# Optimization experiments

Hardware: AMD Instinct MI355X
Metric: run time of the kernel (lower is better)

## Reference

```python
import jax, jax.numpy as jnp
import numpy as np

N_NODES = 100000
EPS_BN = 1e-5


def setup_inputs() -> dict:
    key = jax.random.key(0)
    k1, k2, k3, k4, k5, k6 = jax.random.split(key, 6)
    x = jax.random.normal(k1, (N_NODES, 200), dtype=jnp.float32)
    edge_index = jax.random.randint(k2, (2, 1600000), 0, N_NODES, dtype=jnp.int64)
    # GCNConv params (Glorot-ish scale)
    W = jax.random.normal(k3, (200, 64), dtype=jnp.float32) * (1.0 / np.sqrt(200.0))
    b = jax.random.normal(k4, (64,), dtype=jnp.float32) * 0.01
    # BatchNorm1d affine params
    bn_weight = jax.random.normal(k5, (64,), dtype=jnp.float32) * 0.1 + 1.0
    bn_bias = jax.random.normal(k6, (64,), dtype=jnp.float32) * 0.1
    return {"x": x, "edge_index": edge_index, "W": W, "b": b,
            "bn_weight": bn_weight, "bn_bias": bn_bias}


def _gcn_conv(x, edge_index, W, b):
    n = x.shape[0]
    # linear transform first (PyG GCNConv order): [N, 64]
    xw = x @ W
    # add self-loops
    loop = jnp.arange(n, dtype=edge_index.dtype)
    src = jnp.concatenate([edge_index[0], loop])
    dst = jnp.concatenate([edge_index[1], loop])
    # symmetric normalization: deg over dst (incl. self loops)
    deg = jax.ops.segment_sum(jnp.ones_like(dst, dtype=xw.dtype), dst, num_segments=n)
    dinv = jnp.where(deg > 0, jax.lax.rsqrt(deg), 0.0)
    norm = dinv[src] * dinv[dst]  # [E+N]
    # gather-scale-scatter: out[dst] += norm * xw[src]
    msg = xw[src] * norm[:, None]
    out = jax.ops.segment_sum(msg, dst, num_segments=n)
    return out + b


def reference(x, edge_index, W, b, bn_weight, bn_bias):
    h = _gcn_conv(x, edge_index, W, b)
    h = jax.nn.relu(h)
    # BatchNorm1d in training mode: biased batch statistics over nodes
    mean = jnp.mean(h, axis=0)
    var = jnp.mean(jnp.square(h - mean), axis=0)
    y = (h - mean) * jax.lax.rsqrt(var + EPS_BN) * bn_weight + bn_bias
    return y
```

## Files before the change

### kernel.cpp

```cpp
#include <hip/hip_runtime.h>

#define N_NODES 100000
#define N_EDGES 1600000
#define K_DIM   200
#define C_DIM   64
#define EPS_BN  1e-5f
#define MT      128
#define NKB     25
#define SLICE_U ((size_t)N_NODES * 16)
#define NPX     12500
#define MAXD    48

typedef int      vi4 __attribute__((ext_vector_type(4)));
typedef float    vf4 __attribute__((ext_vector_type(4)));
typedef unsigned vu4 __attribute__((ext_vector_type(4)));

__device__ __forceinline__ ushort f2bf(float f) {
    unsigned u = __float_as_uint(f);
    u = (u + 0x7FFFu + ((u >> 16) & 1u)) >> 16;
    return (ushort)u;
}

__global__ __launch_bounds__(256) void k_fillslot(
        const int* __restrict__ src, const int* __restrict__ dst,
        int* __restrict__ cursor, int* __restrict__ slot) {
    unsigned lo = (blockIdx.x & 7) * NPX;
    int i0 = (blockIdx.x >> 3) * 256 + threadIdx.x;
    int stride = (gridDim.x >> 3) * 256;
    for (int i = i0; i < N_EDGES / 4; i += stride) {
        vi4 d = ((const vi4*)dst)[i];
        vi4 s = ((const vi4*)src)[i];
        bool mx = (unsigned)(d.x - lo) < NPX;
        bool my = (unsigned)(d.y - lo) < NPX;
        bool mz = (unsigned)(d.z - lo) < NPX;
        bool mw = (unsigned)(d.w - lo) < NPX;
        if (mx) { int p = atomicAdd(&cursor[d.x], 1); if (p < MAXD) slot[(size_t)p * N_NODES + d.x] = s.x; }
        if (my) { int p = atomicAdd(&cursor[d.y], 1); if (p < MAXD) slot[(size_t)p * N_NODES + d.y] = s.y; }
        if (mz) { int p = atomicAdd(&cursor[d.z], 1); if (p < MAXD) slot[(size_t)p * N_NODES + d.z] = s.z; }
        if (mw) { int p = atomicAdd(&cursor[d.w], 1); if (p < MAXD) slot[(size_t)p * N_NODES + d.w] = s.w; }
    }
}

__global__ __launch_bounds__(256) void k_gemm2(const float* __restrict__ x,
                                               const float* __restrict__ W,
                                               const int* __restrict__ cursor,
                                               ushort* __restrict__ xsp) {
    __shared__ float xT[8][MT];
    __shared__ float Wt[8][C_DIM];
    int tid = threadIdx.x;
    int tx = tid & 15;
    int ty = tid >> 4;
    int row0 = blockIdx.x * MT;

    int lrow = tid >> 1;
    int lk   = (tid & 1) * 4;
    int grow = row0 + lrow;
    if (grow > N_NODES - 1) grow = N_NODES - 1;
    const float* xp = x + (size_t)grow * K_DIM + lk;
    int wk = tid >> 4;
    int wc = (tid & 15) * 4;

    float acc[8][4];
    #pragma unroll
    for (int i = 0; i < 8; ++i)
        #pragma unroll
        for (int j = 0; j < 4; ++j) acc[i][j] = 0.f;

    float4 xr = *(const float4*)xp;
    float4 wr = {0,0,0,0};
    if (tid < 128) wr = *(const float4*)(W + wk * C_DIM + wc);

    for (int kb = 0; kb < NKB; ++kb) {
        xT[lk + 0][lrow] = xr.x;
        xT[lk + 1][lrow] = xr.y;
        xT[lk + 2][lrow] = xr.z;
        xT[lk + 3][lrow] = xr.w;
        if (tid < 128) *(float4*)&Wt[wk][wc] = wr;
        __syncthreads();
        if (kb < NKB - 1) {
            xr = *(const float4*)(xp + (kb + 1) * 8);
            if (tid < 128) wr = *(const float4*)(W + ((kb + 1) * 8 + wk) * C_DIM + wc);
        }
        #pragma unroll
        for (int k = 0; k < 8; ++k) {
            float4 xa = *(const float4*)&xT[k][ty * 8];
            float4 xb = *(const float4*)&xT[k][ty * 8 + 4];
            float4 wv = *(const float4*)&Wt[k][tx * 4];
            float xv[8] = {xa.x, xa.y, xa.z, xa.w, xb.x, xb.y, xb.z, xb.w};
            #pragma unroll
            for (int i = 0; i < 8; ++i) {
                acc[i][0] = fmaf(xv[i], wv.x, acc[i][0]);
                acc[i][1] = fmaf(xv[i], wv.y, acc[i][1]);
                acc[i][2] = fmaf(xv[i], wv.z, acc[i][2]);
                acc[i][3] = fmaf(xv[i], wv.w, acc[i][3]);
            }
        }
        __syncthreads();
    }
    int sl  = tx >> 2;
    int pos = (tx & 3) * 4;
    #pragma unroll
    for (int i = 0; i < 8; ++i) {
        int r = row0 + ty * 8 + i;
        if (r < N_NODES) {
            float dv = rsqrtf((float)cursor[r] + 1.0f);
            ushort4 o = {f2bf(acc[i][0] * dv), f2bf(acc[i][1] * dv),
                         f2bf(acc[i][2] * dv), f2bf(acc[i][3] * dv)};
            *(ushort4*)(xsp + (size_t)sl * SLICE_U + (size_t)r * 16 + pos) = o;
        }
    }
}

#define UNPK0(u, k) { acc[k] = __uint_as_float((u) << 16); \
                      acc[k+1] = __uint_as_float((u) & 0xFFFF0000u); }
#define UNPKA(u, k) { acc[k] += __uint_as_float((u) << 16); \
                      acc[k+1] += __uint_as_float((u) & 0xFFFF0000u); }
#define ROWACC(aa, cc) { UNPKA(aa.x, 0)  UNPKA(aa.y, 2)  UNPKA(aa.z, 4)  UNPKA(aa.w, 6) \
                         UNPKA(cc.x, 8)  UNPKA(cc.y, 10) UNPKA(cc.z, 12) UNPKA(cc.w, 14) }

__global__ __launch_bounds__(256) void k_gath4(
        const int* __restrict__ slot, const int* __restrict__ cursor,
        const ushort* __restrict__ xsp, const float* __restrict__ b,
        ushort* __restrict__ hp2, float* __restrict__ stats) {
    int tid  = threadIdx.x;
    int lane = tid & 63;
    int widx = tid >> 6;
    int bid  = blockIdx.x;
    int slice = (bid & 7) >> 1;
    int chunk = ((bid >> 3) * 2 + (bid & 1)) * 4 + widx;
    int nchunks = (gridDim.x >> 3) * 8;
    const ushort* xs = xsp + (size_t)slice * SLICE_U;
    const float*  bs = b + slice * 16;
    float s1[16], s2[16];
    #pragma unroll
    for (int i = 0; i < 16; ++i) { s1[i] = 0.f; s2[i] = 0.f; }

    for (int n0 = chunk * 64; n0 < N_NODES; n0 += nchunks * 64) {
        int n = n0 + lane;
        bool act = n < N_NODES;
        int dg = 0;
        float dn = 0.f;
        float acc[16];
        if (act) {
            dg = __builtin_nontemporal_load(cursor + n);
            dn = rsqrtf((float)dg + 1.0f);
            if (dg > MAXD) dg = MAXD;
            const uint4* rp = (const uint4*)(xs + (size_t)n * 16);
            uint4 a = rp[0], c = rp[1];
            UNPK0(a.x, 0)  UNPK0(a.y, 2)  UNPK0(a.z, 4)  UNPK0(a.w, 6)
            UNPK0(c.x, 8)  UNPK0(c.y, 10) UNPK0(c.z, 12) UNPK0(c.w, 14)
        } else {
            #pragma unroll
            for (int i = 0; i < 16; ++i) acc[i] = 0.f;
        }
        const int* sp = slot + n;
        int p = 0;
        for (; p + 4 <= dg; p += 4) {
            int e0 = sp[(size_t)(p + 0) * N_NODES];
            int e1 = sp[(size_t)(p + 1) * N_NODES];
            int e2 = sp[(size_t)(p + 2) * N_NODES];
            int e3 = sp[(size_t)(p + 3) * N_NODES];
            const uint4* q0 = (const uint4*)(xs + (size_t)e0 * 16);
            const uint4* q1 = (const uint4*)(xs + (size_t)e1 * 16);
            const uint4* q2 = (const uint4*)(xs + (size_t)e2 * 16);
            const uint4* q3 = (const uint4*)(xs + (size_t)e3 * 16);
            uint4 a0 = q0[0], c0 = q0[1];
            uint4 a1 = q1[0], c1 = q1[1];
            uint4 a2 = q2[0], c2 = q2[1];
            uint4 a3 = q3[0], c3 = q3[1];
            ROWACC(a0, c0)  ROWACC(a1, c1)  ROWACC(a2, c2)  ROWACC(a3, c3)
        }
        for (; p + 2 <= dg; p += 2) {
            int e0 = sp[(size_t)(p + 0) * N_NODES];
            int e1 = sp[(size_t)(p + 1) * N_NODES];
            const uint4* q0 = (const uint4*)(xs + (size_t)e0 * 16);
            const uint4* q1 = (const uint4*)(xs + (size_t)e1 * 16);
            uint4 a0 = q0[0], c0 = q0[1];
            uint4 a1 = q1[0], c1 = q1[1];
            ROWACC(a0, c0)  ROWACC(a1, c1)
        }
        if (p < dg) {
            int e0 = sp[(size_t)p * N_NODES];
            const uint4* q0 = (const uint4*)(xs + (size_t)e0 * 16);
            uint4 a0 = q0[0], c0 = q0[1];
            ROWACC(a0, c0)
        }
        if (act) {
            unsigned pk[8];
            #pragma unroll
            for (int i2 = 0; i2 < 8; ++i2) {
                float lo = fmaxf(fmaf(dn, acc[2*i2+0], bs[2*i2+0]), 0.f);
                float hi = fmaxf(fmaf(dn, acc[2*i2+1], bs[2*i2+1]), 0.f);
                s1[2*i2+0] += lo; s2[2*i2+0] = fmaf(lo, lo, s2[2*i2+0]);
                s1[2*i2+1] += hi; s2[2*i2+1] = fmaf(hi, hi, s2[2*i2+1]);
                pk[i2] = (unsigned)f2bf(lo) | ((unsigned)f2bf(hi) << 16);
            }
            vu4 w0 = {pk[0], pk[1], pk[2], pk[3]};
            vu4 w1 = {pk[4], pk[5], pk[6], pk[7]};
            ushort* hb = hp2 + ((size_t)slice * N_NODES + (size_t)n) * 16;
            __builtin_nontemporal_store(w0, (vu4*)hb);
            __builtin_nontemporal_store(w1, (vu4*)(hb + 8));
        }
    }

    __shared__ float red[4][32];
    #pragma unroll
    for (int i = 0; i < 16; ++i) {
        float a = s1[i], c = s2[i];
        #pragma unroll
        for (int m = 1; m <= 32; m <<= 1) {
            a += __shfl_xor(a, m);
            c += __shfl_xor(c, m);
        }
        if (lane == 0) { red[widx][i] = a; red[widx][16 + i] = c; }
    }
    __syncthreads();
    if (tid < 32) {
        float v = red[0][tid] + red[1][tid] + red[2][tid] + red[3][tid];
        int ch = slice * 16 + (tid & 15);
        unsafeAtomicAdd(&stats[(tid >> 4) * 64 + ch], v);
    }
}

__global__ __launch_bounds__(256) void k_final_p(
        const ushort* __restrict__ hp2, const float* __restrict__ stats,
        const float* __restrict__ bnw, const float* __restrict__ bnb,
        float* __restrict__ out) {
    int tid = blockIdx.x * 256 + threadIdx.x;
    if (tid >= N_NODES * 8) return;
    int half = tid & 7;
    int n    = tid >> 3;
    int slice = half >> 1, sub = half & 1;
    int cb = slice * 16 + sub * 8;
    float sc[8], sh[8];
    #pragma unroll
    for (int j = 0; j < 8; ++j) {
        int c = cb + j;
        float mean = stats[c] * (1.0f / N_NODES);
        float var  = stats[64 + c] * (1.0f / N_NODES) - mean * mean;
        float s = rsqrtf(var + EPS_BN) * bnw[c];
        sc[j] = s;
        sh[j] = bnb[c] - mean * s;
    }
    vu4 v = __builtin_nontemporal_load(
        (const vu4*)(hp2 + ((size_t)slice * N_NODES + (size_t)n) * 16 + sub * 8));
    vf4 h0, h1;
    h0.x = __uint_as_float(v.x << 16); h0.y = __uint_as_float(v.x & 0xFFFF0000u);
    h0.z = __uint_as_float(v.y << 16); h0.w = __uint_as_float(v.y & 0xFFFF0000u);
    h1.x = __uint_as_float(v.z << 16); h1.y = __uint_as_float(v.z & 0xFFFF0000u);
    h1.z = __uint_as_float(v.w << 16); h1.w = __uint_as_float(v.w & 0xFFFF0000u);
    vf4 o0, o1;
    o0.x = fmaf(h0.x, sc[0], sh[0]); o0.y = fmaf(h0.y, sc[1], sh[1]);
    o0.z = fmaf(h0.z, sc[2], sh[2]); o0.w = fmaf(h0.w, sc[3], sh[3]);
    o1.x = fmaf(h1.x, sc[4], sh[4]); o1.y = fmaf(h1.y, sc[5], sh[5]);
    o1.z = fmaf(h1.z, sc[6], sh[6]); o1.w = fmaf(h1.w, sc[7], sh[7]);
    float* op = out + (size_t)n * C_DIM + cb;
    __builtin_nontemporal_store(o0, (vf4*)op);
    __builtin_nontemporal_store(o1, (vf4*)(op + 4));
}

extern "C" void kernel_launch(void* const* d_in, const int* in_sizes, int n_in,
                              void* d_out, int out_size, void* d_ws, size_t ws_size,
                              hipStream_t stream) {
    const float* x   = (const float*)d_in[0];
    const int*   ei  = (const int*)d_in[1];
    const float* W   = (const float*)d_in[2];
    const float* b   = (const float*)d_in[3];
    const float* bnw = (const float*)d_in[4];
    const float* bnb = (const float*)d_in[5];
    float* out = (float*)d_out;

    const int* src = ei;
    const int* dst = ei + N_EDGES;
    char* ws = (char*)d_ws;

    const size_t SZ_I = 400128;
    const size_t OFF_STAT = SZ_I;
    const size_t OFF_SLOT = SZ_I + 512;
    const size_t OFF_H    = OFF_SLOT + (size_t)N_NODES * MAXD * 4;
    const size_t ZERO_B   = SZ_I + 512;

    ushort* xsp = (ushort*)out;
    const int GEMM_GRID = (N_NODES + MT - 1) / MT;

    int*    cursor = (int*)ws;
    float*  stats  = (float*)(ws + OFF_STAT);
    int*    slot   = (int*)(ws + OFF_SLOT);
    ushort* hp2    = (ushort*)(ws + OFF_H);

    hipMemsetAsync(d_ws, 0, ZERO_B, stream);

    k_fillslot <<<2048, 256, 0, stream>>>(src, dst, cursor, slot);
    k_gemm2    <<<GEMM_GRID, 256, 0, stream>>>(x, W, cursor, xsp);
    k_gath4    <<<3136, 256, 0, stream>>>(slot, cursor, xsp, b, hp2, stats);
    k_final_p  <<<(N_NODES * 8 + 255) / 256, 256, 0, stream>>>(hp2, stats, bnw, bnb, out);
    (void)ws_size;
}
```

Baseline: 201.3 us.

## Fuse edge-slot fill and GEMM into one launch, apply source dinv in gather

The edge-bucketing fill and the x@W GEMM now run as disjoint block ranges of a single kernel, so the compute-bound GEMM can overlap the atomic-heavy fill. This is possible because the GEMM no longer scales rows by the source degree normalization. That scaling moves into the gather, which reads a per-node dinv array built by a new small kernel. The GEMM tile shrinks to 64 rows to give more blocks. The cost is an extra launch plus one extra dinv load and an FMA per gathered edge in the gather.

```diff
diff --git a/kernel.cpp b/kernel.cpp
--- a/kernel.cpp
+++ b/kernel.cpp
@@ -5,11 +5,13 @@
 #define K_DIM   200
 #define C_DIM   64
 #define EPS_BN  1e-5f
-#define MT      128
 #define NKB     25
 #define SLICE_U ((size_t)N_NODES * 16)
 #define NPX     12500
 #define MAXD    48
+#define NFILL   2048
+#define MTG     64
+#define NGEMM   ((N_NODES + MTG - 1) / MTG)
 
 typedef int      vi4 __attribute__((ext_vector_type(4)));
 typedef float    vf4 __attribute__((ext_vector_type(4)));
@@ -21,74 +23,74 @@
     return (ushort)u;
 }
 
-__global__ __launch_bounds__(256) void k_fillslot(
+__global__ __launch_bounds__(256, 8) void k_fillgemm(
         const int* __restrict__ src, const int* __restrict__ dst,
-        int* __restrict__ cursor, int* __restrict__ slot) {
-    unsigned lo = (blockIdx.x & 7) * NPX;
-    int i0 = (blockIdx.x >> 3) * 256 + threadIdx.x;
-    int stride = (gridDim.x >> 3) * 256;
-    for (int i = i0; i < N_EDGES / 4; i += stride) {
-        vi4 d = ((const vi4*)dst)[i];
-        vi4 s = ((const vi4*)src)[i];
-        bool mx = (unsigned)(d.x - lo) < NPX;
-        bool my = (unsigned)(d.y - lo) < NPX;
-        bool mz = (unsigned)(d.z - lo) < NPX;
-        bool mw = (unsigned)(d.w - lo) < NPX;
-        if (mx) { int p = atomicAdd(&cursor[d.x], 1); if (p < MAXD) slot[(size_t)p * N_NODES + d.x] = s.x; }
-        if (my) { int p = atomicAdd(&cursor[d.y], 1); if (p < MAXD) slot[(size_t)p * N_NODES + d.y] = s.y; }
-        if (mz) { int p = atomicAdd(&cursor[d.z], 1); if (p < MAXD) slot[(size_t)p * N_NODES + d.z] = s.z; }
-        if (mw) { int p = atomicAdd(&cursor[d.w], 1); if (p < MAXD) slot[(size_t)p * N_NODES + d.w] = s.w; }
-    }
-}
-
-__global__ __launch_bounds__(256) void k_gemm2(const float* __restrict__ x,
-                                               const float* __restrict__ W,
-                                               const int* __restrict__ cursor,
-                                               ushort* __restrict__ xsp) {
-    __shared__ float xT[8][MT];
+        int* __restrict__ cursor, int* __restrict__ slot,
+        const float* __restrict__ x, const float* __restrict__ W,
+        ushort* __restrict__ xsp) {
+    __shared__ float xT[8][MTG];
     __shared__ float Wt[8][C_DIM];
+    int bid = blockIdx.x;
     int tid = threadIdx.x;
+
+    if (bid < NFILL) {
+        unsigned lo = (bid & 7) * NPX;
+        int i0 = (bid >> 3) * 256 + tid;
+        int stride = (NFILL >> 3) * 256;
+        for (int i = i0; i < N_EDGES / 4; i += stride) {
+            vi4 d = ((const vi4*)dst)[i];
+            vi4 s = ((const vi4*)src)[i];
+            bool mx = (unsigned)(d.x - lo) < NPX;
+            bool my = (unsigned)(d.y - lo) < NPX;
+            bool mz = (unsigned)(d.z - lo) < NPX;
+            bool mw = (unsigned)(d.w - lo) < NPX;
+            if (mx) { int p = atomicAdd(&cursor[d.x], 1); if (p < MAXD) slot[(size_t)p * N_NODES + d.x] = s.x; }
+            if (my) { int p = atomicAdd(&cursor[d.y], 1); if (p < MAXD) slot[(size_t)p * N_NODES + d.y] = s.y; }
+            if (mz) { int p = atomicAdd(&cursor[d.z], 1); if (p < MAXD) slot[(size_t)p * N_NODES + d.z] = s.z; }
+            if (mw) { int p = atomicAdd(&cursor[d.w], 1); if (p < MAXD) slot[(size_t)p * N_NODES + d.w] = s.w; }
+        }
+        return;
+    }
+
+    int gbid = bid - NFILL;
+    int row0 = gbid * MTG;
     int tx = tid & 15;
     int ty = tid >> 4;
-    int row0 = blockIdx.x * MT;
-
-    int lrow = tid >> 1;
-    int lk   = (tid & 1) * 4;
+
+    int lrow = tid >> 2;
+    int lk   = (tid & 3) * 2;
     int grow = row0 + lrow;
     if (grow > N_NODES - 1) grow = N_NODES - 1;
     const float* xp = x + (size_t)grow * K_DIM + lk;
     int wk = tid >> 4;
     int wc = (tid & 15) * 4;
 
-    float acc[8][4];
-    #pragma unroll
-    for (int i = 0; i < 8; ++i)
+    float acc[4][4];
+    #pragma unroll
+    for (int i = 0; i < 4; ++i)
         #pragma unroll
         for (int j = 0; j < 4; ++j) acc[i][j] = 0.f;
 
-    float4 xr = *(const float4*)xp;
+    float2 xr = *(const float2*)xp;
     float4 wr = {0,0,0,0};
     if (tid < 128) wr = *(const float4*)(W + wk * C_DIM + wc);
 
     for (int kb = 0; kb < NKB; ++kb) {
         xT[lk + 0][lrow] = xr.x;
         xT[lk + 1][lrow] = xr.y;
-        xT[lk + 2][lrow] = xr.z;
-        xT[lk + 3][lrow] = xr.w;
         if (tid < 128) *(float4*)&Wt[wk][wc] = wr;
         __syncthreads();
         if (kb < NKB - 1) {
-            xr = *(const float4*)(xp + (kb + 1) * 8);
+            xr = *(const float2*)(xp + (kb + 1) * 8);
             if (tid < 128) wr = *(const float4*)(W + ((kb + 1) * 8 + wk) * C_DIM + wc);
         }
         #pragma unroll
         for (int k = 0; k < 8; ++k) {
-            float4 xa = *(const float4*)&xT[k][ty * 8];
-            float4 xb = *(const float4*)&xT[k][ty * 8 + 4];
+            float4 xa = *(const float4*)&xT[k][ty * 4];
             float4 wv = *(const float4*)&Wt[k][tx * 4];
-            float xv[8] = {xa.x, xa.y, xa.z, xa.w, xb.x, xb.y, xb.z, xb.w};
+            float xv[4] = {xa.x, xa.y, xa.z, xa.w};
             #pragma unroll
-            for (int i = 0; i < 8; ++i) {
+            for (int i = 0; i < 4; ++i) {
                 acc[i][0] = fmaf(xv[i], wv.x, acc[i][0]);
                 acc[i][1] = fmaf(xv[i], wv.y, acc[i][1]);
                 acc[i][2] = fmaf(xv[i], wv.z, acc[i][2]);
@@ -100,28 +102,31 @@
     int sl  = tx >> 2;
     int pos = (tx & 3) * 4;
     #pragma unroll
-    for (int i = 0; i < 8; ++i) {
-        int r = row0 + ty * 8 + i;
+    for (int i = 0; i < 4; ++i) {
+        int r = row0 + ty * 4 + i;
         if (r < N_NODES) {
-            float dv = rsqrtf((float)cursor[r] + 1.0f);
-            ushort4 o = {f2bf(acc[i][0] * dv), f2bf(acc[i][1] * dv),
-                         f2bf(acc[i][2] * dv), f2bf(acc[i][3] * dv)};
+            ushort4 o = {f2bf(acc[i][0]), f2bf(acc[i][1]),
+                         f2bf(acc[i][2]), f2bf(acc[i][3])};
             *(ushort4*)(xsp + (size_t)sl * SLICE_U + (size_t)r * 16 + pos) = o;
         }
     }
 }
 
-#define UNPK0(u, k) { acc[k] = __uint_as_float((u) << 16); \
-                      acc[k+1] = __uint_as_float((u) & 0xFFFF0000u); }
-#define UNPKA(u, k) { acc[k] += __uint_as_float((u) << 16); \
-                      acc[k+1] += __uint_as_float((u) & 0xFFFF0000u); }
-#define ROWACC(aa, cc) { UNPKA(aa.x, 0)  UNPKA(aa.y, 2)  UNPKA(aa.z, 4)  UNPKA(aa.w, 6) \
-                         UNPKA(cc.x, 8)  UNPKA(cc.y, 10) UNPKA(cc.z, 12) UNPKA(cc.w, 14) }
+__global__ void k_dinv(const int* __restrict__ cursor, float* __restrict__ dinv) {
+    int i = blockIdx.x * blockDim.x + threadIdx.x;
+    if (i < N_NODES) dinv[i] = rsqrtf((float)cursor[i] + 1.0f);
+}
+
+#define UNPKA(dv, u, k) { acc[k]   = fmaf(dv, __uint_as_float((u) << 16), acc[k]); \
+                          acc[k+1] = fmaf(dv, __uint_as_float((u) & 0xFFFF0000u), acc[k+1]); }
+#define ROWACC(dv, aa, cc) { UNPKA(dv, aa.x, 0)  UNPKA(dv, aa.y, 2)  UNPKA(dv, aa.z, 4)  UNPKA(dv, aa.w, 6) \
+                             UNPKA(dv, cc.x, 8)  UNPKA(dv, cc.y, 10) UNPKA(dv, cc.z, 12) UNPKA(dv, cc.w, 14) }
 
 __global__ __launch_bounds__(256) void k_gath4(
         const int* __restrict__ slot, const int* __restrict__ cursor,
-        const ushort* __restrict__ xsp, const float* __restrict__ b,
-        ushort* __restrict__ hp2, float* __restrict__ stats) {
+        const float* __restrict__ dinv, const ushort* __restrict__ xsp,
+        const float* __restrict__ b, ushort* __restrict__ hp2,
+        float* __restrict__ stats) {
     int tid  = threadIdx.x;
     int lane = tid & 63;
     int widx = tid >> 6;
@@ -141,17 +146,15 @@
         int dg = 0;
         float dn = 0.f;
         float acc[16];
+        #pragma unroll
+        for (int i = 0; i < 16; ++i) acc[i] = 0.f;
         if (act) {
             dg = __builtin_nontemporal_load(cursor + n);
             dn = rsqrtf((float)dg + 1.0f);
             if (dg > MAXD) dg = MAXD;
             const uint4* rp = (const uint4*)(xs + (size_t)n * 16);
             uint4 a = rp[0], c = rp[1];
-            UNPK0(a.x, 0)  UNPK0(a.y, 2)  UNPK0(a.z, 4)  UNPK0(a.w, 6)
-            UNPK0(c.x, 8)  UNPK0(c.y, 10) UNPK0(c.z, 12) UNPK0(c.w, 14)
-        } else {
-            #pragma unroll
-            for (int i = 0; i < 16; ++i) acc[i] = 0.f;
+            ROWACC(dn, a, c)
         }
         const int* sp = slot + n;
         int p = 0;
@@ -160,6 +163,7 @@
             int e1 = sp[(size_t)(p + 1) * N_NODES];
             int e2 = sp[(size_t)(p + 2) * N_NODES];
             int e3 = sp[(size_t)(p + 3) * N_NODES];
+            float v0 = dinv[e0], v1 = dinv[e1], v2 = dinv[e2], v3 = dinv[e3];
             const uint4* q0 = (const uint4*)(xs + (size_t)e0 * 16);
             const uint4* q1 = (const uint4*)(xs + (size_t)e1 * 16);
             const uint4* q2 = (const uint4*)(xs + (size_t)e2 * 16);
@@ -168,22 +172,25 @@
             uint4 a1 = q1[0], c1 = q1[1];
             uint4 a2 = q2[0], c2 = q2[1];
             uint4 a3 = q3[0], c3 = q3[1];
-            ROWACC(a0, c0)  ROWACC(a1, c1)  ROWACC(a2, c2)  ROWACC(a3, c3)
+            ROWACC(v0, a0, c0)  ROWACC(v1, a1, c1)
+            ROWACC(v2, a2, c2)  ROWACC(v3, a3, c3)
         }
         for (; p + 2 <= dg; p += 2) {
             int e0 = sp[(size_t)(p + 0) * N_NODES];
             int e1 = sp[(size_t)(p + 1) * N_NODES];
+            float v0 = dinv[e0], v1 = dinv[e1];
             const uint4* q0 = (const uint4*)(xs + (size_t)e0 * 16);
             const uint4* q1 = (const uint4*)(xs + (size_t)e1 * 16);
             uint4 a0 = q0[0], c0 = q0[1];
             uint4 a1 = q1[0], c1 = q1[1];
-            ROWACC(a0, c0)  ROWACC(a1, c1)
+            ROWACC(v0, a0, c0)  ROWACC(v1, a1, c1)
         }
         if (p < dg) {
             int e0 = sp[(size_t)p * N_NODES];
+            float v0 = dinv[e0];
             const uint4* q0 = (const uint4*)(xs + (size_t)e0 * 16);
             uint4 a0 = q0[0], c0 = q0[1];
-            ROWACC(a0, c0)
+            ROWACC(v0, a0, c0)
         }
         if (act) {
             unsigned pk[8];
@@ -276,23 +283,24 @@
 
     const size_t SZ_I = 400128;
     const size_t OFF_STAT = SZ_I;
-    const size_t OFF_SLOT = SZ_I + 512;
+    const size_t OFF_DINV = SZ_I + 512;
+    const size_t OFF_SLOT = OFF_DINV + SZ_I;
     const size_t OFF_H    = OFF_SLOT + (size_t)N_NODES * MAXD * 4;
     const size_t ZERO_B   = SZ_I + 512;
 
     ushort* xsp = (ushort*)out;
-    const int GEMM_GRID = (N_NODES + MT - 1) / MT;
 
     int*    cursor = (int*)ws;
     float*  stats  = (float*)(ws + OFF_STAT);
+    float*  dinv   = (float*)(ws + OFF_DINV);
     int*    slot   = (int*)(ws + OFF_SLOT);
     ushort* hp2    = (ushort*)(ws + OFF_H);
 
     hipMemsetAsync(d_ws, 0, ZERO_B, stream);
 
-    k_fillslot <<<2048, 256, 0, stream>>>(src, dst, cursor, slot);
-    k_gemm2    <<<GEMM_GRID, 256, 0, stream>>>(x, W, cursor, xsp);
-    k_gath4    <<<3136, 256, 0, stream>>>(slot, cursor, xsp, b, hp2, stats);
+    k_fillgemm <<<NFILL + NGEMM, 256, 0, stream>>>(src, dst, cursor, slot, x, W, xsp);
+    k_dinv     <<<(N_NODES + 255) / 256, 256, 0, stream>>>(cursor, dinv);
+    k_gath4    <<<3136, 256, 0, stream>>>(slot, cursor, dinv, xsp, b, hp2, stats);
     k_final_p  <<<(N_NODES * 8 + 255) / 256, 256, 0, stream>>>(hp2, stats, bnw, bnb, out);
     (void)ws_size;
 }
```

After: 307.3 us. +52.7%, slower.

## Narrow feature slices from 16 to 8 channels for gather kernel

Applied to the files above, without the earlier changes.

Changes the slice-major bf16 layout of the transformed features from 4 slices of 16 channels to 8 slices of 8 channels. Each gather block now handles one 8-channel slice, so every neighbour row read is a single 16-byte load, and the per-slice working set is halved for better cache residency. In exchange the edge index list and degrees are read twice as many times (once per slice), and the GEMM epilogue and final BN kernel are adjusted to the new layout.

```diff
diff --git a/kernel.cpp b/kernel.cpp
--- a/kernel.cpp
+++ b/kernel.cpp
@@ -7,7 +7,7 @@
 #define EPS_BN  1e-5f
 #define MT      128
 #define NKB     25
-#define SLICE_U ((size_t)N_NODES * 16)
+#define SLICE_U ((size_t)N_NODES * 8)
 #define NPX     12500
 #define MAXD    48
 
@@ -97,8 +97,8 @@
         }
         __syncthreads();
     }
-    int sl  = tx >> 2;
-    int pos = (tx & 3) * 4;
+    int sl  = tx >> 1;
+    int pos = (tx & 1) * 4;
     #pragma unroll
     for (int i = 0; i < 8; ++i) {
         int r = row0 + ty * 8 + i;
@@ -106,7 +106,7 @@
             float dv = rsqrtf((float)cursor[r] + 1.0f);
             ushort4 o = {f2bf(acc[i][0] * dv), f2bf(acc[i][1] * dv),
                          f2bf(acc[i][2] * dv), f2bf(acc[i][3] * dv)};
-            *(ushort4*)(xsp + (size_t)sl * SLICE_U + (size_t)r * 16 + pos) = o;
+            *(ushort4*)(xsp + (size_t)sl * SLICE_U + (size_t)r * 8 + pos) = o;
         }
     }
 }
@@ -115,8 +115,7 @@
                       acc[k+1] = __uint_as_float((u) & 0xFFFF0000u); }
 #define UNPKA(u, k) { acc[k] += __uint_as_float((u) << 16); \
                       acc[k+1] += __uint_as_float((u) & 0xFFFF0000u); }
-#define ROWACC(aa, cc) { UNPKA(aa.x, 0)  UNPKA(aa.y, 2)  UNPKA(aa.z, 4)  UNPKA(aa.w, 6) \
-                         UNPKA(cc.x, 8)  UNPKA(cc.y, 10) UNPKA(cc.z, 12) UNPKA(cc.w, 14) }
+#define ROWACC(aa) { UNPKA(aa.x, 0)  UNPKA(aa.y, 2)  UNPKA(aa.z, 4)  UNPKA(aa.w, 6) }
 
 __global__ __launch_bounds__(256) void k_gath4(
         const int* __restrict__ slot, const int* __restrict__ cursor,
@@ -126,32 +125,30 @@
     int lane = tid & 63;
     int widx = tid >> 6;
     int bid  = blockIdx.x;
-    int slice = (bid & 7) >> 1;
-    int chunk = ((bid >> 3) * 2 + (bid & 1)) * 4 + widx;
-    int nchunks = (gridDim.x >> 3) * 8;
+    int slice = bid & 7;
+    int chunk = (bid >> 3) * 4 + widx;
+    int nchunks = (gridDim.x >> 3) * 4;
     const ushort* xs = xsp + (size_t)slice * SLICE_U;
-    const float*  bs = b + slice * 16;
-    float s1[16], s2[16];
-    #pragma unroll
-    for (int i = 0; i < 16; ++i) { s1[i] = 0.f; s2[i] = 0.f; }
+    const float*  bs = b + slice * 8;
+    float s1[8], s2[8];
+    #pragma unroll
+    for (int i = 0; i < 8; ++i) { s1[i] = 0.f; s2[i] = 0.f; }
 
     for (int n0 = chunk * 64; n0 < N_NODES; n0 += nchunks * 64) {
         int n = n0 + lane;
         bool act = n < N_NODES;
         int dg = 0;
         float dn = 0.f;
-        float acc[16];
+        float acc[8];
         if (act) {
             dg = __builtin_nontemporal_load(cursor + n);
             dn = rsqrtf((float)dg + 1.0f);
             if (dg > MAXD) dg = MAXD;
-            const uint4* rp = (const uint4*)(xs + (size_t)n * 16);
-            uint4 a = rp[0], c = rp[1];
+            uint4 a = *(const uint4*)(xs + (size_t)n * 8);
             UNPK0(a.x, 0)  UNPK0(a.y, 2)  UNPK0(a.z, 4)  UNPK0(a.w, 6)
-            UNPK0(c.x, 8)  UNPK0(c.y, 10) UNPK0(c.z, 12) UNPK0(c.w, 14)
         } else {
             #pragma unroll
-            for (int i = 0; i < 16; ++i) acc[i] = 0.f;
+            for (int i = 0; i < 8; ++i) acc[i] = 0.f;
         }
         const int* sp = slot + n;
         int p = 0;
@@ -160,35 +157,28 @@
             int e1 = sp[(size_t)(p + 1) * N_NODES];
             int e2 = sp[(size_t)(p + 2) * N_NODES];
             int e3 = sp[(size_t)(p + 3) * N_NODES];
-            const uint4* q0 = (const uint4*)(xs + (size_t)e0 * 16);
-            const uint4* q1 = (const uint4*)(xs + (size_t)e1 * 16);
-            const uint4* q2 = (const uint4*)(xs + (size_t)e2 * 16);
-            const uint4* q3 = (const uint4*)(xs + (size_t)e3 * 16);
-            uint4 a0 = q0[0], c0 = q0[1];
-            uint4 a1 = q1[0], c1 = q1[1];
-            uint4 a2 = q2[0], c2 = q2[1];
-            uint4 a3 = q3[0], c3 = q3[1];
-            ROWACC(a0, c0)  ROWACC(a1, c1)  ROWACC(a2, c2)  ROWACC(a3, c3)
+            uint4 a0 = *(const uint4*)(xs + (size_t)e0 * 8);
+            uint4 a1 = *(const uint4*)(xs + (size_t)e1 * 8);
+            uint4 a2 = *(const uint4*)(xs + (size_t)e2 * 8);
+            uint4 a3 = *(const uint4*)(xs + (size_t)e3 * 8);
+            ROWACC(a0)  ROWACC(a1)  ROWACC(a2)  ROWACC(a3)
         }
         for (; p + 2 <= dg; p += 2) {
             int e0 = sp[(size_t)(p + 0) * N_NODES];
             int e1 = sp[(size_t)(p + 1) * N_NODES];
-            const uint4* q0 = (const uint4*)(xs + (size_t)e0 * 16);
-            const uint4* q1 = (const uint4*)(xs + (size_t)e1 * 16);
-            uint4 a0 = q0[0], c0 = q0[1];
-            uint4 a1 = q1[0], c1 = q1[1];
-            ROWACC(a0, c0)  ROWACC(a1, c1)
+            uint4 a0 = *(const uint4*)(xs + (size_t)e0 * 8);
+            uint4 a1 = *(const uint4*)(xs + (size_t)e1 * 8);
+            ROWACC(a0)  ROWACC(a1)
         }
         if (p < dg) {
             int e0 = sp[(size_t)p * N_NODES];
-            const uint4* q0 = (const uint4*)(xs + (size_t)e0 * 16);
-            uint4 a0 = q0[0], c0 = q0[1];
-            ROWACC(a0, c0)
+            uint4 a0 = *(const uint4*)(xs + (size_t)e0 * 8);
+            ROWACC(a0)
         }
         if (act) {
-            unsigned pk[8];
+            unsigned pk[4];
             #pragma unroll
-            for (int i2 = 0; i2 < 8; ++i2) {
+            for (int i2 = 0; i2 < 4; ++i2) {
                 float lo = fmaxf(fmaf(dn, acc[2*i2+0], bs[2*i2+0]), 0.f);
                 float hi = fmaxf(fmaf(dn, acc[2*i2+1], bs[2*i2+1]), 0.f);
                 s1[2*i2+0] += lo; s2[2*i2+0] = fmaf(lo, lo, s2[2*i2+0]);
@@ -196,29 +186,27 @@
                 pk[i2] = (unsigned)f2bf(lo) | ((unsigned)f2bf(hi) << 16);
             }
             vu4 w0 = {pk[0], pk[1], pk[2], pk[3]};
-            vu4 w1 = {pk[4], pk[5], pk[6], pk[7]};
-            ushort* hb = hp2 + ((size_t)slice * N_NODES + (size_t)n) * 16;
-            __builtin_nontemporal_store(w0, (vu4*)hb);
-            __builtin_nontemporal_store(w1, (vu4*)(hb + 8));
-        }
-    }
-
-    __shared__ float red[4][32];
-    #pragma unroll
-    for (int i = 0; i < 16; ++i) {
+            __builtin_nontemporal_store(w0,
+                (vu4*)(hp2 + ((size_t)slice * N_NODES + (size_t)n) * 8));
+        }
+    }
+
+    __shared__ float red[4][16];
+    #pragma unroll
+    for (int i = 0; i < 8; ++i) {
         float a = s1[i], c = s2[i];
         #pragma unroll
         for (int m = 1; m <= 32; m <<= 1) {
             a += __shfl_xor(a, m);
             c += __shfl_xor(c, m);
         }
-        if (lane == 0) { red[widx][i] = a; red[widx][16 + i] = c; }
+        if (lane == 0) { red[widx][i] = a; red[widx][8 + i] = c; }
     }
     __syncthreads();
-    if (tid < 32) {
+    if (tid < 16) {
         float v = red[0][tid] + red[1][tid] + red[2][tid] + red[3][tid];
-        int ch = slice * 16 + (tid & 15);
-        unsafeAtomicAdd(&stats[(tid >> 4) * 64 + ch], v);
+        int ch = slice * 8 + (tid & 7);
+        unsafeAtomicAdd(&stats[(tid >> 3) * 64 + ch], v);
     }
 }
 
@@ -228,10 +216,9 @@
         float* __restrict__ out) {
     int tid = blockIdx.x * 256 + threadIdx.x;
     if (tid >= N_NODES * 8) return;
-    int half = tid & 7;
-    int n    = tid >> 3;
-    int slice = half >> 1, sub = half & 1;
-    int cb = slice * 16 + sub * 8;
+    int slice = tid & 7;
+    int n     = tid >> 3;
+    int cb = slice * 8;
     float sc[8], sh[8];
     #pragma unroll
     for (int j = 0; j < 8; ++j) {
@@ -243,7 +230,7 @@
         sh[j] = bnb[c] - mean * s;
     }
     vu4 v = __builtin_nontemporal_load(
-        (const vu4*)(hp2 + ((size_t)slice * N_NODES + (size_t)n) * 16 + sub * 8));
+        (const vu4*)(hp2 + ((size_t)slice * N_NODES + (size_t)n) * 8));
     vf4 h0, h1;
     h0.x = __uint_as_float(v.x << 16); h0.y = __uint_as_float(v.x & 0xFFFF0000u);
     h0.z = __uint_as_float(v.y << 16); h0.w = __uint_as_float(v.y & 0xFFFF0000u);
```

New measurement: 212.7 us. 1.06x slower.
